# Kernel optimization log

Measured on AMD Instinct MI355X. Metric: run time of the kernel, lower is better.

Reference implementation:

```python
import jax, jax.numpy as jnp
import numpy as np

B, N, C, OUT, E = 2, 512, 256, 256, 18


def setup_inputs() -> dict:
    key = jax.random.key(0)
    ks = jax.random.split(key, 16)
    s = 0.05
    w = lambda k, shape: jax.random.normal(k, shape, jnp.float32) * s
    return dict(
        x=jax.random.normal(ks[0], (B, N, C), jnp.float32),
        adjacency=jax.random.randint(ks[1], (B, N, N), 0, 2, jnp.int32),
        edge_feats=jax.random.normal(ks[2], (B, N, N, E), jnp.float32),
        st_w=w(ks[3], (C, OUT)), st_b=jnp.zeros((OUT,), jnp.float32),
        nt_w=w(ks[4], (C, OUT)), nt_b=jnp.zeros((OUT,), jnp.float32),
        em_w1=w(ks[5], (E, 64)), em_b1=jnp.zeros((64,), jnp.float32),
        em_w2=w(ks[6], (64, 64)), em_b2=jnp.zeros((64,), jnp.float32),
        em_w3=w(ks[7], (64, 32)), em_b3=jnp.zeros((32,), jnp.float32),
        at_w1=w(ks[8], (2 * C + 32, 64)), at_b1=jnp.zeros((64,), jnp.float32),
        at_w2=w(ks[9], (64, 32)), at_b2=jnp.zeros((32,), jnp.float32),
        at_w3=w(ks[10], (32, 1)), at_b3=jnp.zeros((1,), jnp.float32),
        eg_w1=w(ks[11], (C + 32, 64)), eg_b1=jnp.zeros((64,), jnp.float32),
        eg_w2=w(ks[12], (64, OUT)), eg_b2=jnp.zeros((OUT,), jnp.float32),
        cb_w1=w(ks[13], (2 * OUT, OUT)), cb_b1=jnp.zeros((OUT,), jnp.float32),
        cb_w2=w(ks[14], (OUT, OUT)), cb_b2=jnp.zeros((OUT,), jnp.float32),
    )


def reference(x, adjacency, edge_feats,
              st_w, st_b, nt_w, nt_b,
              em_w1, em_b1, em_w2, em_b2, em_w3, em_b3,
              at_w1, at_b1, at_w2, at_b2, at_w3, at_b3,
              eg_w1, eg_b1, eg_w2, eg_b2,
              cb_w1, cb_b1, cb_w2, cb_b2):
    c = x.shape[-1]
    mask = adjacency > 0                      # [B,N,N] neighbor mask (j axis = neighbors of i)
    maskf = mask.astype(x.dtype)
    self_feat = x @ st_w + st_b               # [B,N,OUT]
    nbr = x @ nt_w + nt_b                     # [B,N,OUT] transformed neighbor feats
    # edge MLP 18->64->64->32
    pe = jax.nn.relu(edge_feats @ em_w1 + em_b1)
    pe = jax.nn.relu(pe @ em_w2 + em_b2)
    pe = jax.nn.relu(pe @ em_w3 + em_b3)      # [B,N,N,32]
    # attention MLP on concat(x_i, x_j, pe): split first layer to avoid [B,N,N,2C+32]
    a_i = x @ at_w1[:c]                       # [B,N,64]
    a_j = x @ at_w1[c:2 * c]                  # [B,N,64]
    a_e = pe @ at_w1[2 * c:]                  # [B,N,N,64]
    h = jax.nn.relu(a_i[:, :, None, :] + a_j[:, None, :, :] + a_e + at_b1)
    h = jax.nn.relu(h @ at_w2 + at_b2)        # [B,N,N,32]
    scores = (h @ at_w3)[..., 0] + at_b3[0]   # [B,N,N]
    scores = jnp.where(mask, scores, jnp.asarray(-1e9, x.dtype))
    attn = jax.nn.softmax(scores, axis=-1) * maskf  # softmax over neighbor set of each i
    # edge gate on concat(x_j, pe): split first layer
    g = jax.nn.relu((x @ eg_w1[:c])[:, None, :, :] + pe @ eg_w1[c:] + eg_b1)
    g = jax.nn.sigmoid(g @ eg_w2 + eg_b2)     # [B,N,N,OUT]
    gated = g * nbr[:, None, :, :]            # [B,N,N,OUT]
    msg = jnp.einsum('bij,bijc->bic', attn, gated)
    has_nbr = mask.any(axis=-1)[..., None].astype(x.dtype)
    msg = msg * has_nbr                        # nodes with no neighbors get zero message
    comb = jnp.concatenate([self_feat, msg], axis=-1)
    out = jax.nn.relu(comb @ cb_w1 + cb_b1) @ cb_w2 + cb_b2
    return out
```

## Files before the change

### kernel.cpp

```cpp
#include <hip/hip_runtime.h>

#define BB 2
#define NN 512
#define CC 256
#define OO 256
#define EE 18

#define OFF_SF   0
#define OFF_NBR  (BB*NN*OO)
#define OFF_AI   (OFF_NBR + BB*NN*OO)
#define OFF_AJ   (OFF_AI + BB*NN*64)
#define OFF_EGX  (OFF_AJ + BB*NN*64)
#define OFF_MSG  (OFF_EGX + BB*NN*64)
#define OFF_WN   OFF_MSG
#define OFF_W1   OFF_AI
#define OFF_W2   OFF_AJ

typedef float f32x4 __attribute__((ext_vector_type(4)));
typedef __bf16 bf16x8 __attribute__((ext_vector_type(8)));

__device__ __forceinline__ unsigned short f2bf(float f) {
  unsigned u = __float_as_uint(f);
  u += 0x7fffu + ((u >> 16) & 1u);
  return (unsigned short)(u >> 16);
}
__device__ __forceinline__ unsigned pk2(float a, float b) {
  return (unsigned)f2bf(a) | ((unsigned)f2bf(b) << 16);
}
__device__ __forceinline__ int swzc(int chunk, int row) {
  return (chunk & ~7) | ((chunk ^ row) & 7);
}

__device__ __forceinline__ f32x4 mfma_bf16(uint4 a, uint4 b, f32x4 c) {
  return __builtin_amdgcn_mfma_f32_16x16x32_bf16(
      __builtin_bit_cast(bf16x8, a), __builtin_bit_cast(bf16x8, b), c, 0, 0, 0);
}

__global__ __launch_bounds__(256) void k_prep_w(
    const float* __restrict__ em_w1, const float* __restrict__ em_w2,
    const float* __restrict__ em_w3, const float* __restrict__ at_w1,
    const float* __restrict__ at_w2, const float* __restrict__ eg_w1,
    const float* __restrict__ eg_w2,
    const float* __restrict__ st_w,  const float* __restrict__ nt_w,
    unsigned char* __restrict__ img, float* __restrict__ ws)
{
  int bid = blockIdx.x;
  if (bid < 120) {
    int idx = bid * 256 + threadIdx.x;
    const float* src; int KV, RO, k, l, ldw;
    if (idx < 2048)       { src = em_w1;          KV = 18; RO = 0;     k = idx>>6;  l = idx&63;  ldw = 64; }
    else if (idx < 6144)  { src = em_w2;          KV = 64; RO = 8192;  int e = idx-2048;  k = e>>6; l = e&63;  ldw = 64; }
    else if (idx < 8192)  { src = em_w3;          KV = 64; RO = 16384; int e = idx-6144;  k = e>>5; l = e&31;  ldw = 32; }
    else if (idx < 10240) { src = at_w1 + 512*64; KV = 32; RO = 20480; int e = idx-8192;  k = e>>6; l = e&63;  ldw = 64; }
    else if (idx < 12288) { src = at_w2;          KV = 64; RO = 28672; int e = idx-10240; k = e>>5; l = e&31;  ldw = 32; }
    else if (idx < 14336) { src = eg_w1 + 256*64; KV = 32; RO = 32768; int e = idx-12288; k = e>>6; l = e&63;  ldw = 64; }
    else                  { src = eg_w2;          KV = 64; RO = 40960; int e = idx-14336; k = e>>8; l = e&255; ldw = 256; }
    float v = (k < KV) ? src[(size_t)k*ldw + l] : 0.f;
    *(unsigned short*)(img + RO + l*128 + ((((k>>3) ^ (l&7))) << 4) + ((k&7) << 1)) = f2bf(v);
  } else {
    unsigned char* dst = (unsigned char*)(ws + OFF_WN);
    int idx = (bid - 120) * 256 + threadIdx.x;
    int col = idx >> 5, ch = idx & 31;
    const float* src; int ld, c;
    if (col < 256)      { src = st_w;           ld = 256; c = col; }
    else if (col < 512) { src = nt_w;           ld = 256; c = col - 256; }
    else if (col < 576) { src = at_w1;          ld = 64;  c = col - 512; }
    else if (col < 640) { src = at_w1 + 256*64; ld = 64;  c = col - 576; }
    else                { src = eg_w1;          ld = 64;  c = col - 640; }
    float e[8];
    #pragma unroll
    for (int q = 0; q < 8; ++q) e[q] = src[(size_t)(ch*8+q)*ld + c];
    uint4 v = make_uint4(pk2(e[0],e[1]), pk2(e[2],e[3]), pk2(e[4],e[5]), pk2(e[6],e[7]));
    *(uint4*)(dst + (size_t)col*512 + swzc(ch, col)*16) = v;
  }
}

__global__ __launch_bounds__(256) void k_prep_out(
    const float* __restrict__ cb_w1, const float* __restrict__ cb_w2,
    float* __restrict__ ws)
{
  int bid = blockIdx.x;
  if (bid < 64) {
    unsigned char* dst = (unsigned char*)(ws + OFF_W1);
    int idx = bid * 256 + threadIdx.x;
    int col = idx >> 6, ch = idx & 63;
    float e[8];
    #pragma unroll
    for (int q = 0; q < 8; ++q) e[q] = cb_w1[(size_t)(ch*8+q)*256 + col];
    uint4 v = make_uint4(pk2(e[0],e[1]), pk2(e[2],e[3]), pk2(e[4],e[5]), pk2(e[6],e[7]));
    *(uint4*)(dst + (size_t)col*1024 + swzc(ch, col)*16) = v;
  } else {
    unsigned char* dst = (unsigned char*)(ws + OFF_W2);
    int idx = (bid - 64) * 256 + threadIdx.x;
    int col = idx >> 5, ch = idx & 31;
    float e[8];
    #pragma unroll
    for (int q = 0; q < 8; ++q) e[q] = cb_w2[(size_t)(ch*8+q)*256 + col];
    uint4 v = make_uint4(pk2(e[0],e[1]), pk2(e[2],e[3]), pk2(e[4],e[5]), pk2(e[6],e[7]));
    *(uint4*)(dst + (size_t)col*512 + swzc(ch, col)*16) = v;
  }
}

__global__ __launch_bounds__(256) void k_node(
    const float* __restrict__ x,
    const float* __restrict__ st_b, const float* __restrict__ nt_b,
    float* __restrict__ ws)
{
  __shared__ __align__(16) unsigned char sA[64*512];
  const int t = threadIdx.x;
  const int c0 = blockIdx.x * 64, g0 = blockIdx.y * 64;

  for (int idx = t; idx < 64*64; idx += 256) {
    int row = idx >> 6, kq = idx & 63;
    float4 v = *(const float4*)(x + (size_t)(g0 + row)*CC + kq*4);
    uint2 p; p.x = pk2(v.x, v.y); p.y = pk2(v.z, v.w);
    *(uint2*)(sA + row*512 + swzc(kq >> 1, row)*16 + (kq & 1)*8) = p;
  }
  __syncthreads();

  const int wid = t >> 6, lane = t & 63, l4 = lane >> 4, l16 = lane & 15;
  const unsigned char* WN = (const unsigned char*)(ws + OFF_WN);

  uint4 af[8];
  {
    int row = wid*16 + l16;
    #pragma unroll
    for (int f = 0; f < 8; ++f)
      af[f] = *(const uint4*)(sA + row*512 + swzc(l4 + 4*f, row)*16);
  }

  #pragma unroll
  for (int ct = 0; ct < 4; ++ct) {
    int gcol = c0 + ct*16 + l16;
    f32x4 acc = {0.f, 0.f, 0.f, 0.f};
    #pragma unroll
    for (int f = 0; f < 8; ++f) {
      uint4 bfr = *(const uint4*)(WN + (size_t)gcol*512 + swzc(l4 + 4*f, gcol)*16);
      acc = mfma_bf16(af[f], bfr, acc);
    }
    int gr0 = g0 + wid*16 + l4*4;
    int bb = gr0 >> 9, n0 = gr0 & 511;
    if (gcol < 256) {
      float bz = st_b[gcol];
      #pragma unroll
      for (int r = 0; r < 4; ++r) ws[OFF_SF + (size_t)(gr0+r)*OO + gcol] = acc[r] + bz;
    } else if (gcol < 512) {
      int c = gcol - 256;
      float bz = nt_b[c];
      f32x4 v = {acc[0]+bz, acc[1]+bz, acc[2]+bz, acc[3]+bz};
      *(f32x4*)(ws + OFF_NBR + ((size_t)bb*256 + c)*512 + n0) = v;
    } else if (gcol < 576) {
      #pragma unroll
      for (int r = 0; r < 4; ++r) ws[OFF_AI + (size_t)(gr0+r)*64 + (gcol-512)] = acc[r];
    } else if (gcol < 640) {
      int c = gcol - 576;
      *(f32x4*)(ws + OFF_AJ + ((size_t)bb*64 + c)*512 + n0) = acc;
    } else {
      int c = gcol - 640;
      *(f32x4*)(ws + OFF_EGX + ((size_t)bb*64 + c)*512 + n0) = acc;
    }
  }
}

__global__ __launch_bounds__(512, 2) void k_edge(
    const int*   __restrict__ adj,
    const float* __restrict__ ef_g,
    const unsigned char* __restrict__ wimg,
    const float* __restrict__ em_b1g, const float* __restrict__ em_b2g,
    const float* __restrict__ em_b3g,
    const float* __restrict__ at_b1g, const float* __restrict__ at_b2g,
    const float* __restrict__ at_w3g, const float* __restrict__ at_b3g,
    const float* __restrict__ eg_b1g, const float* __restrict__ eg_b2g,
    float* __restrict__ ws)
{
  __shared__ __align__(16) unsigned char s_act[512*128];
  __shared__ float s_bem1[64], s_bem2[64], s_bem3[32];
  __shared__ float s_t1init[64], s_bat2[32], s_w3[32];
  __shared__ float s_beg1[64], s_beg2[256];
  __shared__ __align__(16) float s_sc[512];
  __shared__ float s_red[8];
  __shared__ float s_msg[8][256];

  const int t = threadIdx.x;
  const int i = blockIdx.x, b = blockIdx.y;
  const int wid = t >> 6, lane = t & 63, l4 = lane >> 4, l16 = lane & 15;
  const int R = wid * 64;

  const unsigned char* Wem1 = wimg;
  const unsigned char* Wem2 = wimg + 8192;
  const unsigned char* Wem3 = wimg + 16384;
  const unsigned char* Wat1 = wimg + 20480;
  const unsigned char* Wat2 = wimg + 28672;
  const unsigned char* Weg1 = wimg + 32768;
  const unsigned char* Weg2 = wimg + 40960;

  if (t < 64) {
    s_bem1[t]   = em_b1g[t];
    s_bem2[t]   = em_b2g[t];
    s_t1init[t] = ws[OFF_AI + (size_t)(b*NN + i)*64 + t] + at_b1g[t];
    s_beg1[t]   = eg_b1g[t];
  } else if (t < 96)  { s_bem3[t-64]  = em_b3g[t-64]; }
  else if (t < 128)   { s_bat2[t-96]  = at_b2g[t-96]; }
  else if (t < 160)   { s_w3[t-128]   = at_w3g[t-128]; }
  if (t < 256) s_beg2[t] = eg_b2g[t];
  const float atb3 = at_b3g[0];

  const float maskf = adj[(size_t)(b*NN + i)*NN + t] > 0 ? 1.f : 0.f;

  {
    const int j = t;
    const float* efp = ef_g + ((size_t)(b*NN + i)*NN + j) * EE;
    float e[32];
    #pragma unroll
    for (int k = 0; k < 9; ++k) { float2 v2 = *(const float2*)(efp + 2*k); e[2*k] = v2.x; e[2*k+1] = v2.y; }
    #pragma unroll
    for (int k = EE; k < 32; ++k) e[k] = 0.f;
    #pragma unroll
    for (int c = 0; c < 4; ++c) {
      uint4 u = make_uint4(pk2(e[c*8+0],e[c*8+1]), pk2(e[c*8+2],e[c*8+3]),
                           pk2(e[c*8+4],e[c*8+5]), pk2(e[c*8+6],e[c*8+7]));
      *(uint4*)(s_act + j*128 + ((c ^ (j & 7)) << 4)) = u;
    }
  }
  __syncthreads();

  auto loadA = [&](int rb, int f) -> uint4 {
    int rw = rb + l16;
    return *(const uint4*)(s_act + rw*128 + (((l4 + 4*f) ^ (rw & 7)) << 4));
  };
  auto loadB = [&](const unsigned char* w, int ct, int f) -> uint4 {
    int rw = ct*16 + l16;
    return *(const uint4*)(w + rw*128 + (((l4 + 4*f) ^ (rw & 7)) << 4));
  };
  auto storeCR = [&](int rb, int ct, const f32x4& c) {
    int col = ct*16 + l16;
    #pragma unroll
    for (int r = 0; r < 4; ++r) {
      int rw = rb + l4*4 + r;
      *(unsigned short*)(s_act + rw*128 + (((col >> 3) ^ (rw & 7)) << 4) + ((col & 7) << 1))
          = f2bf(fmaxf(c[r], 0.f));
    }
  };

  const float* ajT  = ws + OFF_AJ  + (size_t)b*64*512;
  const float* egT  = ws + OFF_EGX + (size_t)b*64*512;
  const float* nbrT = ws + OFF_NBR + (size_t)b*256*512;

  uint4 peA[4];

  {
    uint4 B[4];
    #pragma unroll
    for (int ct = 0; ct < 4; ++ct) B[ct] = loadB(Wem1, ct, 0);
    #pragma unroll
    for (int st = 0; st < 4; ++st) {
      int rb = R + st*16;
      uint4 a = loadA(rb, 0);
      #pragma unroll
      for (int ct = 0; ct < 4; ++ct) {
        float bz = s_bem1[ct*16 + l16];
        f32x4 c = {bz, bz, bz, bz};
        c = mfma_bf16(a, B[ct], c);
        storeCR(rb, ct, c);
      }
    }
  }
  {
    uint4 B[4][2];
    #pragma unroll
    for (int ct = 0; ct < 4; ++ct) { B[ct][0] = loadB(Wem2, ct, 0); B[ct][1] = loadB(Wem2, ct, 1); }
    #pragma unroll
    for (int st = 0; st < 4; ++st) {
      int rb = R + st*16;
      uint4 a0 = loadA(rb, 0), a1 = loadA(rb, 1);
      #pragma unroll
      for (int ct = 0; ct < 4; ++ct) {
        float bz = s_bem2[ct*16 + l16];
        f32x4 c = {bz, bz, bz, bz};
        c = mfma_bf16(a0, B[ct][0], c);
        c = mfma_bf16(a1, B[ct][1], c);
        storeCR(rb, ct, c);
      }
    }
  }
  {
    uint4 B[2][2];
    #pragma unroll
    for (int ct = 0; ct < 2; ++ct) { B[ct][0] = loadB(Wem3, ct, 0); B[ct][1] = loadB(Wem3, ct, 1); }
    #pragma unroll
    for (int st = 0; st < 4; ++st) {
      int rb = R + st*16;
      uint4 a0 = loadA(rb, 0), a1 = loadA(rb, 1);
      #pragma unroll
      for (int ct = 0; ct < 2; ++ct) {
        float bz = s_bem3[ct*16 + l16];
        f32x4 c = {bz, bz, bz, bz};
        c = mfma_bf16(a0, B[ct][0], c);
        c = mfma_bf16(a1, B[ct][1], c);
        storeCR(rb, ct, c);
      }
      peA[st] = loadA(rb, 0);
    }
  }
  {
    uint4 B[4];
    #pragma unroll
    for (int ct = 0; ct < 4; ++ct) B[ct] = loadB(Wat1, ct, 0);
    #pragma unroll
    for (int st = 0; st < 4; ++st) {
      int rb = R + st*16;
      #pragma unroll
      for (int ct = 0; ct < 4; ++ct) {
        int col = ct*16 + l16;
        f32x4 av = *(const f32x4*)(ajT + (size_t)col*512 + rb + l4*4);
        float ti = s_t1init[col];
        f32x4 c = {ti + av[0], ti + av[1], ti + av[2], ti + av[3]};
        c = mfma_bf16(peA[st], B[ct], c);
        storeCR(rb, ct, c);
      }
    }
  }
  {
    uint4 B[2][2];
    #pragma unroll
    for (int ct = 0; ct < 2; ++ct) { B[ct][0] = loadB(Wat2, ct, 0); B[ct][1] = loadB(Wat2, ct, 1); }
    #pragma unroll
    for (int st = 0; st < 4; ++st) {
      int rb = R + st*16;
      uint4 a0 = loadA(rb, 0), a1 = loadA(rb, 1);
      float b0 = s_bat2[l16], b1v = s_bat2[16 + l16];
      f32x4 c0 = {b0, b0, b0, b0}, c1 = {b1v, b1v, b1v, b1v};
      c0 = mfma_bf16(a0, B[0][0], c0); c0 = mfma_bf16(a1, B[0][1], c0);
      c1 = mfma_bf16(a0, B[1][0], c1); c1 = mfma_bf16(a1, B[1][1], c1);
      float w3a = s_w3[l16], w3b = s_w3[16 + l16];
      #pragma unroll
      for (int r = 0; r < 4; ++r) {
        float val = fmaxf(c0[r], 0.f)*w3a + fmaxf(c1[r], 0.f)*w3b;
        val += __shfl_xor(val, 1); val += __shfl_xor(val, 2);
        val += __shfl_xor(val, 4); val += __shfl_xor(val, 8);
        if (l16 == 0) s_sc[rb + l4*4 + r] = val + atb3;
      }
    }
  }
  {
    uint4 B[4];
    #pragma unroll
    for (int ct = 0; ct < 4; ++ct) B[ct] = loadB(Weg1, ct, 0);
    #pragma unroll
    for (int st = 0; st < 4; ++st) {
      int rb = R + st*16;
      #pragma unroll
      for (int ct = 0; ct < 4; ++ct) {
        int col = ct*16 + l16;
        f32x4 ev = *(const f32x4*)(egT + (size_t)col*512 + rb + l4*4);
        float bg = s_beg1[col];
        f32x4 c = {bg + ev[0], bg + ev[1], bg + ev[2], bg + ev[3]};
        c = mfma_bf16(peA[st], B[ct], c);
        storeCR(rb, ct, c);
      }
    }
  }
  __syncthreads();

  {
    float v  = maskf > 0.f ? s_sc[t] : -1e9f;
    float m = v;
    #pragma unroll
    for (int d = 1; d < 64; d <<= 1) m = fmaxf(m, __shfl_xor(m, d));
    if (lane == 0) s_red[wid] = m;
    __syncthreads();
    float mx = s_red[0];
    #pragma unroll
    for (int w = 1; w < 8; ++w) mx = fmaxf(mx, s_red[w]);
    float p = maskf > 0.f ? __expf(v - mx) : 0.f;
    float sm = p;
    #pragma unroll
    for (int d = 1; d < 64; d <<= 1) sm += __shfl_xor(sm, d);
    __syncthreads();
    if (lane == 0) s_red[wid] = sm;
    __syncthreads();
    float den = 0.f;
    #pragma unroll
    for (int w = 0; w < 8; ++w) den += s_red[w];
    float inv = den > 0.f ? 1.f/den : 0.f;
    s_sc[t] = p * inv;
  }
  __syncthreads();

  {
    uint4 gA[4][2];
    #pragma unroll
    for (int st = 0; st < 4; ++st) { gA[st][0] = loadA(R + st*16, 0); gA[st][1] = loadA(R + st*16, 1); }

    for (int ct = 0; ct < 16; ++ct) {
      uint4 B0 = loadB(Weg2, ct, 0), B1 = loadB(Weg2, ct, 1);
      int col = ct*16 + l16;
      float bz = s_beg2[col];
      const float* nbrc = nbrT + (size_t)col*512 + R + l4*4;
      float msgp = 0.f;
      #pragma unroll
      for (int st = 0; st < 4; ++st) {
        f32x4 nv = *(const f32x4*)(nbrc + st*16);
        f32x4 at = *(const f32x4*)(&s_sc[R + st*16 + l4*4]);
        f32x4 c = {bz, bz, bz, bz};
        c = mfma_bf16(gA[st][0], B0, c);
        c = mfma_bf16(gA[st][1], B1, c);
        #pragma unroll
        for (int r = 0; r < 4; ++r) {
          float g = __builtin_amdgcn_rcpf(1.f + __expf(-c[r]));
          msgp += g * at[r] * nv[r];
        }
      }
      msgp += __shfl_xor(msgp, 16);
      msgp += __shfl_xor(msgp, 32);
      if (lane < 16) s_msg[wid][ct*16 + lane] = msgp;
    }
  }
  __syncthreads();
  if (t < 256) {
    float s = 0.f;
    #pragma unroll
    for (int w = 0; w < 8; ++w) s += s_msg[w][t];
    ws[OFF_MSG + (size_t)(b*NN + i)*OO + t] = s;
  }
}

__global__ __launch_bounds__(256) void k_out(
    const float* __restrict__ cb_b1, const float* __restrict__ cb_b2,
    const float* __restrict__ ws, float* __restrict__ out)
{
  __shared__ __align__(16) unsigned char sA[16*1024];
  __shared__ __align__(16) unsigned char sT[16*512];
  const int t = threadIdx.x;
  const int g0 = blockIdx.x * 16;

  for (int idx = t; idx < 16*128; idx += 256) {
    int row = idx >> 7, kq = idx & 127;
    const float* src = (kq < 64)
        ? ws + OFF_SF  + (size_t)(g0 + row)*OO + kq*4
        : ws + OFF_MSG + (size_t)(g0 + row)*OO + (kq - 64)*4;
    float4 v = *(const float4*)src;
    uint2 p; p.x = pk2(v.x, v.y); p.y = pk2(v.z, v.w);
    *(uint2*)(sA + row*1024 + swzc(kq >> 1, row)*16 + (kq & 1)*8) = p;
  }
  __syncthreads();

  const int wid = t >> 6, lane = t & 63, l4 = lane >> 4, l16 = lane & 15;
  const unsigned char* W1 = (const unsigned char*)(ws + OFF_W1);
  const unsigned char* W2 = (const unsigned char*)(ws + OFF_W2);

  {
    uint4 af[16];
    #pragma unroll
    for (int f = 0; f < 16; ++f)
      af[f] = *(const uint4*)(sA + l16*1024 + swzc(l4 + 4*f, l16)*16);
    #pragma unroll
    for (int c = 0; c < 4; ++c) {
      int col = wid*64 + c*16 + l16;
      float bz = cb_b1[col];
      f32x4 acc = {bz, bz, bz, bz};
      #pragma unroll
      for (int f = 0; f < 16; ++f) {
        uint4 bfr = *(const uint4*)(W1 + (size_t)col*1024 + swzc(l4 + 4*f, col)*16);
        acc = mfma_bf16(af[f], bfr, acc);
      }
      #pragma unroll
      for (int r = 0; r < 4; ++r) {
        int row = l4*4 + r;
        *(unsigned short*)(sT + row*512 + swzc(col >> 3, row)*16 + (col & 7)*2)
            = f2bf(fmaxf(acc[r], 0.f));
      }
    }
  }
  __syncthreads();

  {
    uint4 tf[8];
    #pragma unroll
    for (int f = 0; f < 8; ++f)
      tf[f] = *(const uint4*)(sT + l16*512 + swzc(l4 + 4*f, l16)*16);
    #pragma unroll
    for (int c = 0; c < 4; ++c) {
      int col = wid*64 + c*16 + l16;
      float bz = cb_b2[col];
      f32x4 acc = {bz, bz, bz, bz};
      #pragma unroll
      for (int f = 0; f < 8; ++f) {
        uint4 bfr = *(const uint4*)(W2 + (size_t)col*512 + swzc(l4 + 4*f, col)*16);
        acc = mfma_bf16(tf[f], bfr, acc);
      }
      #pragma unroll
      for (int r = 0; r < 4; ++r)
        out[(size_t)(g0 + l4*4 + r)*OO + col] = acc[r];
    }
  }
}

extern "C" void kernel_launch(void* const* d_in, const int* in_sizes, int n_in,
                              void* d_out, int out_size, void* d_ws, size_t ws_size,
                              hipStream_t stream) {
  const float* x     = (const float*)d_in[0];
  const int*   adj   = (const int*)  d_in[1];
  const float* ef    = (const float*)d_in[2];
  const float* st_w  = (const float*)d_in[3];
  const float* st_b  = (const float*)d_in[4];
  const float* nt_w  = (const float*)d_in[5];
  const float* nt_b  = (const float*)d_in[6];
  const float* em_w1 = (const float*)d_in[7];
  const float* em_b1 = (const float*)d_in[8];
  const float* em_w2 = (const float*)d_in[9];
  const float* em_b2 = (const float*)d_in[10];
  const float* em_w3 = (const float*)d_in[11];
  const float* em_b3 = (const float*)d_in[12];
  const float* at_w1 = (const float*)d_in[13];
  const float* at_b1 = (const float*)d_in[14];
  const float* at_w2 = (const float*)d_in[15];
  const float* at_b2 = (const float*)d_in[16];
  const float* at_w3 = (const float*)d_in[17];
  const float* at_b3 = (const float*)d_in[18];
  const float* eg_w1 = (const float*)d_in[19];
  const float* eg_b1 = (const float*)d_in[20];
  const float* eg_w2 = (const float*)d_in[21];
  const float* eg_b2 = (const float*)d_in[22];
  const float* cb_w1 = (const float*)d_in[23];
  const float* cb_b1 = (const float*)d_in[24];
  const float* cb_w2 = (const float*)d_in[25];
  const float* cb_b2 = (const float*)d_in[26];
  float* ws  = (float*)d_ws;
  float* out = (float*)d_out;
  unsigned char* wimg = (unsigned char*)d_out;

  k_prep_w<<<dim3(208), dim3(256), 0, stream>>>(em_w1, em_w2, em_w3, at_w1, at_w2,
      eg_w1, eg_w2, st_w, nt_w, wimg, ws);
  k_node<<<dim3(11, 16), dim3(256), 0, stream>>>(x, st_b, nt_b, ws);
  k_edge<<<dim3(NN, BB), dim3(512), 0, stream>>>(adj, ef, wimg,
      em_b1, em_b2, em_b3, at_b1, at_b2, at_w3, at_b3, eg_b1, eg_b2, ws);
  k_prep_out<<<dim3(96), dim3(256), 0, stream>>>(cb_w1, cb_w2, ws);
  k_out<<<dim3(64), dim3(256), 0, stream>>>(cb_b1, cb_b2, ws, out);
}
```

Baseline: 171.9 us.

## Swap MFMA operands to produce transposed tiles with packed bf16 stores

The MLP layers in the edge kernel now put the weight fragment in the A slot and the activations in the B slot, so each lane holds four consecutive output columns for one edge row. That allows packed bf16 conversion (v_cvt_pk_bf16_f32) and one 8-byte LDS store per tile instead of four scalar 2-byte stores, plus vectorized bias loads from LDS. The node projection kernel is changed the same way, so the AJ/EGX intermediates are stored row-major and read as float4 per row. The final score reduction now uses cross-quad shuffles instead of a 16-lane butterfly. The transposed NBR write in the prep kernel becomes scalar strided stores, which may cost a little there.

Result: faster. 141.0 us (median of 4 runs) (-18.0%).

```diff
diff --git a/kernel.cpp b/kernel.cpp
--- a/kernel.cpp
+++ b/kernel.cpp
@@ -26,6 +26,11 @@
 }
 __device__ __forceinline__ unsigned pk2(float a, float b) {
   return (unsigned)f2bf(a) | ((unsigned)f2bf(b) << 16);
+}
+__device__ __forceinline__ unsigned cvtpk(float a, float b) {
+  unsigned r;
+  asm("v_cvt_pk_bf16_f32 %0, %1, %2" : "=v"(r) : "v"(a), "v"(b));
+  return r;
 }
 __device__ __forceinline__ int swzc(int chunk, int row) {
   return (chunk & ~7) | ((chunk ^ row) & 7);
@@ -129,35 +134,35 @@
       af[f] = *(const uint4*)(sA + row*512 + swzc(l4 + 4*f, row)*16);
   }
 
+  const int grow = g0 + wid*16 + l16;
+  const int bb = grow >> 9, n0 = grow & 511;
+
   #pragma unroll
   for (int ct = 0; ct < 4; ++ct) {
-    int gcol = c0 + ct*16 + l16;
+    int gcolL = c0 + ct*16 + l16;
     f32x4 acc = {0.f, 0.f, 0.f, 0.f};
     #pragma unroll
     for (int f = 0; f < 8; ++f) {
-      uint4 bfr = *(const uint4*)(WN + (size_t)gcol*512 + swzc(l4 + 4*f, gcol)*16);
-      acc = mfma_bf16(af[f], bfr, acc);
-    }
-    int gr0 = g0 + wid*16 + l4*4;
-    int bb = gr0 >> 9, n0 = gr0 & 511;
-    if (gcol < 256) {
-      float bz = st_b[gcol];
-      #pragma unroll
-      for (int r = 0; r < 4; ++r) ws[OFF_SF + (size_t)(gr0+r)*OO + gcol] = acc[r] + bz;
-    } else if (gcol < 512) {
-      int c = gcol - 256;
-      float bz = nt_b[c];
-      f32x4 v = {acc[0]+bz, acc[1]+bz, acc[2]+bz, acc[3]+bz};
-      *(f32x4*)(ws + OFF_NBR + ((size_t)bb*256 + c)*512 + n0) = v;
-    } else if (gcol < 576) {
-      #pragma unroll
-      for (int r = 0; r < 4; ++r) ws[OFF_AI + (size_t)(gr0+r)*64 + (gcol-512)] = acc[r];
-    } else if (gcol < 640) {
-      int c = gcol - 576;
-      *(f32x4*)(ws + OFF_AJ + ((size_t)bb*64 + c)*512 + n0) = acc;
+      uint4 wfr = *(const uint4*)(WN + (size_t)gcolL*512 + swzc(l4 + 4*f, gcolL)*16);
+      acc = mfma_bf16(wfr, af[f], acc);
+    }
+    int gcol0 = c0 + ct*16 + l4*4;
+    if (gcol0 < 256) {
+      f32x4 bz = *(const f32x4*)(st_b + gcol0);
+      f32x4 v = acc + bz;
+      *(f32x4*)(ws + OFF_SF + (size_t)grow*OO + gcol0) = v;
+    } else if (gcol0 < 512) {
+      int c = gcol0 - 256;
+      f32x4 bz = *(const f32x4*)(nt_b + c);
+      #pragma unroll
+      for (int r = 0; r < 4; ++r)
+        ws[OFF_NBR + ((size_t)bb*256 + c + r)*512 + n0] = acc[r] + bz[r];
+    } else if (gcol0 < 576) {
+      *(f32x4*)(ws + OFF_AI + (size_t)grow*64 + (gcol0-512)) = acc;
+    } else if (gcol0 < 640) {
+      *(f32x4*)(ws + OFF_AJ + (size_t)grow*64 + (gcol0-576)) = acc;
     } else {
-      int c = gcol - 640;
-      *(f32x4*)(ws + OFF_EGX + ((size_t)bb*64 + c)*512 + n0) = acc;
+      *(f32x4*)(ws + OFF_EGX + (size_t)grow*64 + (gcol0-640)) = acc;
     }
   }
 }
@@ -174,9 +179,9 @@
     float* __restrict__ ws)
 {
   __shared__ __align__(16) unsigned char s_act[512*128];
-  __shared__ float s_bem1[64], s_bem2[64], s_bem3[32];
-  __shared__ float s_t1init[64], s_bat2[32], s_w3[32];
-  __shared__ float s_beg1[64], s_beg2[256];
+  __shared__ __align__(16) float s_bem1[64], s_bem2[64], s_bem3[32];
+  __shared__ __align__(16) float s_t1init[64], s_bat2[32], s_w3[32];
+  __shared__ __align__(16) float s_beg1[64], s_beg2[256];
   __shared__ __align__(16) float s_sc[512];
   __shared__ float s_red[8];
   __shared__ float s_msg[8][256];
@@ -232,131 +237,130 @@
     int rw = ct*16 + l16;
     return *(const uint4*)(w + rw*128 + (((l4 + 4*f) ^ (rw & 7)) << 4));
   };
-  auto storeCR = [&](int rb, int ct, const f32x4& c) {
-    int col = ct*16 + l16;
-    #pragma unroll
-    for (int r = 0; r < 4; ++r) {
-      int rw = rb + l4*4 + r;
-      *(unsigned short*)(s_act + rw*128 + (((col >> 3) ^ (rw & 7)) << 4) + ((col & 7) << 1))
-          = f2bf(fmaxf(c[r], 0.f));
-    }
+  auto storeCT = [&](int rb, int ct, const f32x4& c) {
+    int rw = rb + l16;
+    int col0 = ct*16 + l4*4;
+    uint2 v;
+    v.x = cvtpk(fmaxf(c[0], 0.f), fmaxf(c[1], 0.f));
+    v.y = cvtpk(fmaxf(c[2], 0.f), fmaxf(c[3], 0.f));
+    *(uint2*)(s_act + rw*128 + swzc(col0 >> 3, rw)*16 + (col0 & 7)*2) = v;
   };
 
-  const float* ajT  = ws + OFF_AJ  + (size_t)b*64*512;
-  const float* egT  = ws + OFF_EGX + (size_t)b*64*512;
+  const float* ajR  = ws + OFF_AJ  + (size_t)b*NN*64;
+  const float* egR  = ws + OFF_EGX + (size_t)b*NN*64;
   const float* nbrT = ws + OFF_NBR + (size_t)b*256*512;
 
   uint4 peA[4];
 
   {
-    uint4 B[4];
-    #pragma unroll
-    for (int ct = 0; ct < 4; ++ct) B[ct] = loadB(Wem1, ct, 0);
+    uint4 W[4];
+    #pragma unroll
+    for (int ct = 0; ct < 4; ++ct) W[ct] = loadB(Wem1, ct, 0);
     #pragma unroll
     for (int st = 0; st < 4; ++st) {
       int rb = R + st*16;
       uint4 a = loadA(rb, 0);
       #pragma unroll
       for (int ct = 0; ct < 4; ++ct) {
-        float bz = s_bem1[ct*16 + l16];
-        f32x4 c = {bz, bz, bz, bz};
-        c = mfma_bf16(a, B[ct], c);
-        storeCR(rb, ct, c);
-      }
-    }
-  }
-  {
-    uint4 B[4][2];
-    #pragma unroll
-    for (int ct = 0; ct < 4; ++ct) { B[ct][0] = loadB(Wem2, ct, 0); B[ct][1] = loadB(Wem2, ct, 1); }
+        f32x4 c = *(const f32x4*)&s_bem1[ct*16 + l4*4];
+        c = mfma_bf16(W[ct], a, c);
+        storeCT(rb, ct, c);
+      }
+    }
+  }
+  {
+    uint4 W[4][2];
+    #pragma unroll
+    for (int ct = 0; ct < 4; ++ct) { W[ct][0] = loadB(Wem2, ct, 0); W[ct][1] = loadB(Wem2, ct, 1); }
     #pragma unroll
     for (int st = 0; st < 4; ++st) {
       int rb = R + st*16;
       uint4 a0 = loadA(rb, 0), a1 = loadA(rb, 1);
       #pragma unroll
       for (int ct = 0; ct < 4; ++ct) {
-        float bz = s_bem2[ct*16 + l16];
-        f32x4 c = {bz, bz, bz, bz};
-        c = mfma_bf16(a0, B[ct][0], c);
-        c = mfma_bf16(a1, B[ct][1], c);
-        storeCR(rb, ct, c);
-      }
-    }
-  }
-  {
-    uint4 B[2][2];
-    #pragma unroll
-    for (int ct = 0; ct < 2; ++ct) { B[ct][0] = loadB(Wem3, ct, 0); B[ct][1] = loadB(Wem3, ct, 1); }
+        f32x4 c = *(const f32x4*)&s_bem2[ct*16 + l4*4];
+        c = mfma_bf16(W[ct][0], a0, c);
+        c = mfma_bf16(W[ct][1], a1, c);
+        storeCT(rb, ct, c);
+      }
+    }
+  }
+  {
+    uint4 W[2][2];
+    #pragma unroll
+    for (int ct = 0; ct < 2; ++ct) { W[ct][0] = loadB(Wem3, ct, 0); W[ct][1] = loadB(Wem3, ct, 1); }
     #pragma unroll
     for (int st = 0; st < 4; ++st) {
       int rb = R + st*16;
       uint4 a0 = loadA(rb, 0), a1 = loadA(rb, 1);
       #pragma unroll
       for (int ct = 0; ct < 2; ++ct) {
-        float bz = s_bem3[ct*16 + l16];
-        f32x4 c = {bz, bz, bz, bz};
-        c = mfma_bf16(a0, B[ct][0], c);
-        c = mfma_bf16(a1, B[ct][1], c);
-        storeCR(rb, ct, c);
+        f32x4 c = *(const f32x4*)&s_bem3[ct*16 + l4*4];
+        c = mfma_bf16(W[ct][0], a0, c);
+        c = mfma_bf16(W[ct][1], a1, c);
+        storeCT(rb, ct, c);
       }
       peA[st] = loadA(rb, 0);
     }
   }
   {
-    uint4 B[4];
-    #pragma unroll
-    for (int ct = 0; ct < 4; ++ct) B[ct] = loadB(Wat1, ct, 0);
+    uint4 W[4];
+    #pragma unroll
+    for (int ct = 0; ct < 4; ++ct) W[ct] = loadB(Wat1, ct, 0);
     #pragma unroll
     for (int st = 0; st < 4; ++st) {
       int rb = R + st*16;
+      int j = rb + l16;
       #pragma unroll
       for (int ct = 0; ct < 4; ++ct) {
-        int col = ct*16 + l16;
-        f32x4 av = *(const f32x4*)(ajT + (size_t)col*512 + rb + l4*4);
-        float ti = s_t1init[col];
-        f32x4 c = {ti + av[0], ti + av[1], ti + av[2], ti + av[3]};
-        c = mfma_bf16(peA[st], B[ct], c);
-        storeCR(rb, ct, c);
-      }
-    }
-  }
-  {
-    uint4 B[2][2];
-    #pragma unroll
-    for (int ct = 0; ct < 2; ++ct) { B[ct][0] = loadB(Wat2, ct, 0); B[ct][1] = loadB(Wat2, ct, 1); }
+        int col0 = ct*16 + l4*4;
+        f32x4 ti = *(const f32x4*)&s_t1init[col0];
+        f32x4 av = *(const f32x4*)(ajR + (size_t)j*64 + col0);
+        f32x4 c = ti + av;
+        c = mfma_bf16(W[ct], peA[st], c);
+        storeCT(rb, ct, c);
+      }
+    }
+  }
+  {
+    uint4 W[2][2];
+    #pragma unroll
+    for (int ct = 0; ct < 2; ++ct) { W[ct][0] = loadB(Wat2, ct, 0); W[ct][1] = loadB(Wat2, ct, 1); }
     #pragma unroll
     for (int st = 0; st < 4; ++st) {
       int rb = R + st*16;
       uint4 a0 = loadA(rb, 0), a1 = loadA(rb, 1);
-      float b0 = s_bat2[l16], b1v = s_bat2[16 + l16];
-      f32x4 c0 = {b0, b0, b0, b0}, c1 = {b1v, b1v, b1v, b1v};
-      c0 = mfma_bf16(a0, B[0][0], c0); c0 = mfma_bf16(a1, B[0][1], c0);
-      c1 = mfma_bf16(a0, B[1][0], c1); c1 = mfma_bf16(a1, B[1][1], c1);
-      float w3a = s_w3[l16], w3b = s_w3[16 + l16];
+      f32x4 c0 = *(const f32x4*)&s_bat2[l4*4];
+      f32x4 c1 = *(const f32x4*)&s_bat2[16 + l4*4];
+      c0 = mfma_bf16(W[0][0], a0, c0); c0 = mfma_bf16(W[0][1], a1, c0);
+      c1 = mfma_bf16(W[1][0], a0, c1); c1 = mfma_bf16(W[1][1], a1, c1);
+      float val = 0.f;
       #pragma unroll
       for (int r = 0; r < 4; ++r) {
-        float val = fmaxf(c0[r], 0.f)*w3a + fmaxf(c1[r], 0.f)*w3b;
-        val += __shfl_xor(val, 1); val += __shfl_xor(val, 2);
-        val += __shfl_xor(val, 4); val += __shfl_xor(val, 8);
-        if (l16 == 0) s_sc[rb + l4*4 + r] = val + atb3;
-      }
-    }
-  }
-  {
-    uint4 B[4];
-    #pragma unroll
-    for (int ct = 0; ct < 4; ++ct) B[ct] = loadB(Weg1, ct, 0);
+        val += fmaxf(c0[r], 0.f)*s_w3[l4*4 + r];
+        val += fmaxf(c1[r], 0.f)*s_w3[16 + l4*4 + r];
+      }
+      val += __shfl_xor(val, 16);
+      val += __shfl_xor(val, 32);
+      if (l4 == 0) s_sc[rb + l16] = val + atb3;
+    }
+  }
+  {
+    uint4 W[4];
+    #pragma unroll
+    for (int ct = 0; ct < 4; ++ct) W[ct] = loadB(Weg1, ct, 0);
     #pragma unroll
     for (int st = 0; st < 4; ++st) {
       int rb = R + st*16;
+      int j = rb + l16;
       #pragma unroll
       for (int ct = 0; ct < 4; ++ct) {
-        int col = ct*16 + l16;
-        f32x4 ev = *(const f32x4*)(egT + (size_t)col*512 + rb + l4*4);
-        float bg = s_beg1[col];
-        f32x4 c = {bg + ev[0], bg + ev[1], bg + ev[2], bg + ev[3]};
-        c = mfma_bf16(peA[st], B[ct], c);
-        storeCR(rb, ct, c);
+        int col0 = ct*16 + l4*4;
+        f32x4 bg = *(const f32x4*)&s_beg1[col0];
+        f32x4 ev = *(const f32x4*)(egR + (size_t)j*64 + col0);
+        f32x4 c = bg + ev;
+        c = mfma_bf16(W[ct], peA[st], c);
+        storeCT(rb, ct, c);
       }
     }
   }
```
